# Kernel optimization log

Hardware: AMD Instinct MI355X
Metric: run time of the kernel (lower is better)

Reference implementation:

```python
import jax, jax.numpy as jnp
import numpy as np

B, N, IN_DIM, HID, K = 32, 512, 1024, 512, 3
ALPHA = 0.2  # leaky_relu negative slope
NEG = -9e15


def setup_inputs() -> dict:
    key = jax.random.key(0)
    ks = jax.random.split(key, 7)
    hidden_states = jax.random.normal(ks[0], (B, N, IN_DIM), jnp.float32)
    adj = (jax.random.uniform(ks[1], (B, 3, N, N)) < 0.05).astype(jnp.float32)
    W_all = jax.random.normal(ks[2], (3, K, IN_DIM, HID), jnp.float32) * 0.02
    a_all = jax.random.normal(ks[3], (3, K, 2 * HID, 1), jnp.float32) * 0.02
    wawa_w = jax.random.normal(ks[4], (HID, 100), jnp.float32) * 0.05
    wawa_b = jnp.zeros((100,), jnp.float32)
    ctx_w = jax.random.normal(ks[5], (100, 1), jnp.float32) * 0.05
    return {"hidden_states": hidden_states, "adj": adj, "W_all": W_all,
            "a_all": a_all, "wawa_w": wawa_w, "wawa_b": wawa_b, "ctx_w": ctx_w}


def _gat(adj_m, x, W, a):
    # e_ij = leaky_relu(cat[h_i, h_j] @ a) == leaky_relu(h_i@a1 + h_j@a2)
    h = jnp.einsum('bnf,fh->bnh', x, W)           # [B,N,HID]
    f1 = jnp.einsum('bnh,ho->bno', h, a[:HID])    # [B,N,1]
    f2 = jnp.einsum('bnh,ho->bno', h, a[HID:])    # [B,N,1]
    e = jax.nn.leaky_relu(f1 + jnp.swapaxes(f2, 1, 2), negative_slope=ALPHA)  # [B,N,N]
    att = jnp.where(adj_m > 0, e, NEG)
    att = jax.nn.softmax(att, axis=2)
    return jnp.einsum('bnm,bmh->bnh', att, h)


def reference(hidden_states, adj, W_all, a_all, wawa_w, wawa_b, ctx_w):
    adj_a, adj_b, adj_c = adj[:, 0], adj[:, 1], adj[:, 2]
    pa, pb, pc = adj_a, adj_b, adj_c  # matmuls(A, k) = A^(k+1)
    hs = []
    for layer in range(K):
        if layer > 0:
            pa = jnp.matmul(pa, adj_a)
            pb = jnp.matmul(pb, adj_b)
            pc = jnp.matmul(pc, adj_c)
        h_layer = (_gat(pa, hidden_states, W_all[0, layer], a_all[0, layer])
                   + _gat(pb, hidden_states, W_all[1, layer], a_all[1, layer])
                   + _gat(pc, hidden_states, W_all[2, layer], a_all[2, layer]))
        hs.append(h_layer)
    # attention-based combination over the K orders
    s = [jnp.einsum('bnc,co->bno', jnp.tanh(jnp.einsum('bnh,hc->bnc', h, wawa_w) + wawa_b), ctx_w)
         for h in hs]                              # each [B,N,1]
    vs = jax.nn.softmax(jnp.concatenate(s, axis=2), axis=2)  # [B,N,K]
    h_stack = jnp.stack(hs, axis=2)                # [B,N,K,HID]
    return jnp.sum(vs[..., None] * h_stack, axis=2)  # [B,N,HID]
```

## Files before the change

kernel.cpp:

```cpp
#include <hip/hip_runtime.h>
#include <hip/hip_bf16.h>

typedef short v8s __attribute__((ext_vector_type(8)));
typedef float v4f __attribute__((ext_vector_type(4)));
typedef unsigned long long u64;

#define ALPHA 0.2f

__device__ inline unsigned short f32_bf16(float x){
    unsigned int u = __float_as_uint(x);
    unsigned int r = (u + 0x7fffu + ((u >> 16) & 1u)) >> 16;
    return (unsigned short)r;
}
__device__ inline float bf16_f32(unsigned short s){
    return __uint_as_float(((unsigned int)s) << 16);
}
__device__ inline v4f mfma16(v8s a, v8s b, v4f c){
    return __builtin_amdgcn_mfma_f32_16x16x32_bf16(a, b, c, 0, 0, 0);
}
__device__ inline void gload16(const unsigned short* g, short* l){
    __builtin_amdgcn_global_load_lds((const __attribute__((address_space(1))) unsigned int*)g,
                                     (__attribute__((address_space(3))) unsigned int*)l,
                                     16, 0, 0);
}


__global__ void k_convert_x(const float* __restrict__ x, v8s* __restrict__ out, int n8){
    int i = blockIdx.x * 256 + threadIdx.x;
    if (i >= n8) return;
    const float4* p = (const float4*)x + (size_t)i * 2;
    float4 a = p[0], b = p[1];
    v8s r;
    r[0] = (short)f32_bf16(a.x); r[1] = (short)f32_bf16(a.y);
    r[2] = (short)f32_bf16(a.z); r[3] = (short)f32_bf16(a.w);
    r[4] = (short)f32_bf16(b.x); r[5] = (short)f32_bf16(b.y);
    r[6] = (short)f32_bf16(b.z); r[7] = (short)f32_bf16(b.w);
    out[i] = r;
}

__global__ void k_transpose_w(const float* __restrict__ W, unsigned short* __restrict__ Wt){
    __shared__ float tile[32][33];
    int g = blockIdx.z, k0 = blockIdx.x * 32, h0 = blockIdx.y * 32;
    int tx = threadIdx.x, ty = threadIdx.y;
    #pragma unroll
    for (int i = 0; i < 4; ++i)
        tile[ty + i*8][tx] = W[((size_t)g*1024 + k0 + ty + i*8)*512 + h0 + tx];
    __syncthreads();
    #pragma unroll
    for (int i = 0; i < 4; ++i){
        int h = ty + i*8;
        Wt[((size_t)g*512 + h0 + h)*1024 + k0 + tx] = f32_bf16(tile[tx][h]);
    }
}

__global__ void k_wawat(const float* __restrict__ w, unsigned short* __restrict__ wt){
    int i = blockIdx.x * 256 + threadIdx.x;
    if (i >= 128 * 512) return;
    int c = i >> 9, k = i & 511;
    wt[i] = (c < 100) ? f32_bf16(w[k*100 + c]) : (unsigned short)0;
}


__global__ __launch_bounds__(256) void k_bits(const float* __restrict__ adj,
                                              u64* __restrict__ bits){
    int row = blockIdx.x * 4 + (threadIdx.x >> 6);
    int t = row >> 14, b = (row >> 9) & 31, i = row & 511;
    const float* src = adj + (((size_t)b*3 + t)*512 + i)*512;
    int lane = threadIdx.x & 63;
    #pragma unroll
    for (int w = 0; w < 8; ++w){
        u64 word = __ballot(src[w*64 + lane] > 0.5f);
        if (lane == 0) bits[(size_t)row*8 + w] = word;
    }
}

__global__ __launch_bounds__(256) void k_boolmm(const u64* __restrict__ prev,
                                                const u64* __restrict__ base,
                                                u64* __restrict__ out){
    int row = blockIdx.x * 256 + threadIdx.x;
    if (row >= 49152) return;
    int tb = row >> 9;
    const u64* pr = prev + (size_t)row * 8;
    const u64* bb = base + ((size_t)tb << 9) * 8;
    ulonglong2 a0 = {0,0}, a1 = {0,0}, a2 = {0,0}, a3 = {0,0};
    #pragma unroll
    for (int w = 0; w < 8; ++w){
        u64 m = pr[w];
        const u64* bw = bb + (size_t)(w << 6) * 8;
        while (m){
            int k = __builtin_ctzll(m);
            m &= m - 1;
            const ulonglong2* br = (const ulonglong2*)(bw + (size_t)k * 8);
            ulonglong2 b0 = br[0], b1 = br[1], b2 = br[2], b3 = br[3];
            a0.x |= b0.x; a0.y |= b0.y;
            a1.x |= b1.x; a1.y |= b1.y;
            a2.x |= b2.x; a2.y |= b2.y;
            a3.x |= b3.x; a3.y |= b3.y;
        }
    }
    ulonglong2* op = (ulonglong2*)(out + (size_t)row * 8);
    op[0] = a0; op[1] = a1; op[2] = a2; op[3] = a3;
}

__global__ __launch_bounds__(256, 4) void k_gemm_h(
    const unsigned short* __restrict__ Wt, const unsigned short* __restrict__ Xb,
    unsigned short* __restrict__ Ht, const float* __restrict__ aall,
    float* __restrict__ f1p, float* __restrict__ f2p, int l)
{
    __shared__ __align__(16) short As[128*32];
    __shared__ __align__(16) short Bs[128*32];
    const int bn = blockIdx.x, bm = blockIdx.y, t = blockIdx.z;
    const int g = t*3 + l;
    const int tid = threadIdx.x;
    const int lane = tid & 63, wave = tid >> 6;
    const int wr = wave >> 1, wc = wave & 1;
    const int fr = lane & 15, fq = lane >> 4;
    const int slot = fq ^ (fr & 3) ^ ((fr >> 2) & 3);

    const int srow = tid >> 2, sw = tid & 3;
    const int gw = sw ^ (srow & 3) ^ ((srow >> 2) & 3);
    const unsigned short* Ap = Wt + ((size_t)g*512 + (size_t)bm*128 + srow)*1024 + gw*8;
    const unsigned short* Bp = Xb + ((size_t)bn*128 + srow)*1024 + gw*8;
    short* AsW = As + wave*512;
    short* BsW = Bs + wave*512;

    v4f acc[4][4] = {};

    for (int kt = 0; kt < 32; ++kt){
        const unsigned short* a0 = Ap + kt*32;
        const unsigned short* b0 = Bp + kt*32;
        gload16(a0,           AsW);
        gload16(a0 + 64*1024, AsW + 2048);
        gload16(b0,           BsW);
        gload16(b0 + 64*1024, BsW + 2048);
        __syncthreads();
        v8s af[4], bf[4];
        #pragma unroll
        for (int i = 0; i < 4; ++i) af[i] = *(const v8s*)&As[(wr*64 + i*16 + fr)*32 + slot*8];
        #pragma unroll
        for (int i = 0; i < 4; ++i) bf[i] = *(const v8s*)&Bs[(wc*64 + i*16 + fr)*32 + slot*8];
        #pragma unroll
        for (int i = 0; i < 4; ++i)
            #pragma unroll
            for (int j = 0; j < 4; ++j)
                acc[i][j] = mfma16(af[i], bf[j], acc[i][j]);
        __syncthreads();
    }
    #pragma unroll
    for (int i = 0; i < 4; ++i){
        const int h = bm*128 + wr*64 + i*16 + fq*4;
        #pragma unroll
        for (int j = 0; j < 4; ++j){
            const int mc = bn*128 + wc*64 + j*16 + fr;
            unsigned short* dst = Ht + ((size_t)t*512 + h)*16384 + mc;
            #pragma unroll
            for (int rg = 0; rg < 4; ++rg)
                dst[(size_t)rg*16384] = f32_bf16(acc[i][j][rg]);
        }
    }
    const float* a1 = aall + ((size_t)t*3 + l)*1024;
    const float* a2 = a1 + 512;
    float s1[4] = {0.f,0.f,0.f,0.f}, s2[4] = {0.f,0.f,0.f,0.f};
    #pragma unroll
    for (int i = 0; i < 4; ++i){
        #pragma unroll
        for (int rg = 0; rg < 4; ++rg){
            const int h = bm*128 + wr*64 + i*16 + fq*4 + rg;
            const float c1 = a1[h], c2 = a2[h];
            #pragma unroll
            for (int j = 0; j < 4; ++j){
                s1[j] += acc[i][j][rg]*c1;
                s2[j] += acc[i][j][rg]*c2;
            }
        }
    }
    #pragma unroll
    for (int j = 0; j < 4; ++j){
        s1[j] += __shfl_xor(s1[j], 16); s1[j] += __shfl_xor(s1[j], 32);
        s2[j] += __shfl_xor(s2[j], 16); s2[j] += __shfl_xor(s2[j], 32);
    }
    float* scr = (float*)As;
    __syncthreads();
    if (fq == 0){
        #pragma unroll
        for (int j = 0; j < 4; ++j){
            scr[(((wr*2 + wc)*4 + j)*16 + fr)*2 + 0] = s1[j];
            scr[(((wr*2 + wc)*4 + j)*16 + fr)*2 + 1] = s2[j];
        }
    }
    __syncthreads();
    if (tid < 256){
        const int which = tid & 1, fr2 = (tid >> 1) & 15, j2 = (tid >> 5) & 3,
                  wc2 = (tid >> 7) & 1;
        const float v = scr[(((0*2 + wc2)*4 + j2)*16 + fr2)*2 + which]
                      + scr[(((1*2 + wc2)*4 + j2)*16 + fr2)*2 + which];
        const int m = bn*128 + wc2*64 + j2*16 + fr2;
        float* dst = which ? f2p : f1p;
        dst[((size_t)bm*3 + t)*16384 + m] = v;
    }
}

__global__ __launch_bounds__(256) void k_f1red(
    const float* __restrict__ f1p, const float* __restrict__ f2p,
    float* __restrict__ f1, float* __restrict__ f2)
{
    int idx = blockIdx.x * 256 + threadIdx.x;
    if (idx >= 49152) return;
    float s1 = 0.f, s2 = 0.f;
    #pragma unroll
    for (int bm = 0; bm < 4; ++bm){
        int t = idx >> 14, m = idx & 16383;
        s1 += f1p[((size_t)bm*3 + t)*16384 + m];
        s2 += f2p[((size_t)bm*3 + t)*16384 + m];
    }
    f1[idx] = s1; f2[idx] = s2;
}

__device__ inline void softmax_row(int t, int b, int rt, int r, int q,
    const float* __restrict__ f1a, const float* __restrict__ f2a,
    const u64* __restrict__ maskP, float* p)
{
    const float f1v = f1a[t*16384 + b*512 + rt*64 + r];
    const u64 mw = maskP[(((size_t)t*32 + b)*512 + rt*64 + r)*8 + q];
    const float4* f2p = (const float4*)(f2a + t*16384 + b*512 + q*64);
    float sm = 0.f;
    #pragma unroll
    for (int w = 0; w < 16; ++w){
        float4 f4 = f2p[w];
        #pragma unroll
        for (int u2 = 0; u2 < 4; ++u2){
            int u = w*4 + u2;
            float e = f1v + ((const float*)&f4)[u2];
            e = (e >= 0.f) ? e : ALPHA*e;
            float pe = ((mw >> u) & 1ull) ? __expf(e) : 0.f;
            p[u] = pe; sm += pe;
        }
    }
    sm += __shfl_xor(sm, 1);
    sm += __shfl_xor(sm, 2);
    sm += __shfl_xor(sm, 4);
    const float rinv = 1.f / (sm + 1e-30f);
    #pragma unroll
    for (int u = 0; u < 64; ++u) p[u] *= rinv;
}

__device__ inline void store_att(short* __restrict__ attbuf, int r, int q,
                                 const float* p)
{
    #pragma unroll
    for (int j8 = 0; j8 < 8; ++j8){
        v8s pk;
        #pragma unroll
        for (int u = 0; u < 8; ++u) pk[u] = (short)f32_bf16(p[j8*8 + u]);
        const int cs = q*8 + (j8 ^ q);
        *(v8s*)&attbuf[r*520 + cs*8] = pk;
    }
}

#define PV_LOAD(buf, kknum) { \
    _Pragma("unroll") \
    for (int j = 0; j < 4; ++j) \
        buf[j] = *(const v8s*)(Hb + (size_t)(wave*64 + j*16 + fr)*16384 + (kknum)*32 + fq*8); }

#define PV_MFMA(buf) { \
    _Pragma("unroll") \
    for (int i = 0; i < 4; ++i) \
        _Pragma("unroll") \
        for (int j = 0; j < 4; ++j) \
            acc[i][j] = mfma16(af[i], buf[j], acc[i][j]); }

#define PV_BODY(ATT) { \
    _Pragma("unroll") \
    for (int kk = 0; kk < 16; ++kk){ \
        const int nx = kk + 3; \
        if (nx < 16){ \
            if (nx % 4 == 0)      { PV_LOAD(bva, nx) } \
            else if (nx % 4 == 1) { PV_LOAD(bvb, nx) } \
            else if (nx % 4 == 2) { PV_LOAD(bvc, nx) } \
            else                  { PV_LOAD(bvd, nx) } \
        } \
        v8s af[4]; \
        const int cb = kk*4 + fq; \
        const int cs = (cb & 56) | ((cb & 7) ^ ((cb >> 3) & 7)); \
        _Pragma("unroll") \
        for (int i = 0; i < 4; ++i) \
            af[i] = *(const v8s*)&ATT[(i*16 + fr)*520 + cs*8]; \
        if (kk % 4 == 0)      { PV_MFMA(bva) } \
        else if (kk % 4 == 1) { PV_MFMA(bvb) } \
        else if (kk % 4 == 2) { PV_MFMA(bvc) } \
        else                  { PV_MFMA(bvd) } \
    } }

__global__ __launch_bounds__(512, 2) void k_att_pv(
    const unsigned short* __restrict__ Ht,
    const float* __restrict__ f1a, const float* __restrict__ f2a,
    const u64* __restrict__ maskP,
    unsigned short* __restrict__ hlb)
{
    __shared__ __align__(16) short att0[64*520];
    __shared__ __align__(16) short att1[64*520];
    const int tid = threadIdx.x;
    const int lane = tid & 63, wave = tid >> 6;
    const int b = blockIdx.x, rt = blockIdx.y;
    const int r = tid >> 3, q = tid & 7;
    const int fr = lane & 15, fq = lane >> 4;
    v4f acc[4][4] = {};
    float p[64];
    v8s bva[4], bvb[4], bvc[4], bvd[4];

    const unsigned short* Hb = Ht + (size_t)b*512;

    PV_LOAD(bva, 0); PV_LOAD(bvb, 1); PV_LOAD(bvc, 2);
    softmax_row(0, b, rt, r, q, f1a, f2a, maskP, p);
    store_att(att0, r, q, p);
    __syncthreads();

    softmax_row(1, b, rt, r, q, f1a, f2a, maskP, p);
    store_att(att1, r, q, p);
    PV_BODY(att0);
    __syncthreads();

    Hb += (size_t)512*16384;
    PV_LOAD(bva, 0); PV_LOAD(bvb, 1); PV_LOAD(bvc, 2);
    softmax_row(2, b, rt, r, q, f1a, f2a, maskP, p);
    store_att(att0, r, q, p);
    PV_BODY(att1);
    __syncthreads();

    Hb += (size_t)512*16384;
    PV_LOAD(bva, 0); PV_LOAD(bvb, 1); PV_LOAD(bvc, 2);
    PV_BODY(att0);

    #pragma unroll
    for (int i = 0; i < 4; ++i){
        const int row = rt*64 + i*16 + fq*4;
        #pragma unroll
        for (int j = 0; j < 4; ++j){
            const int col = wave*64 + j*16 + fr;
            unsigned short* d1 = hlb + ((size_t)b*512 + row)*512 + col;
            #pragma unroll
            for (int rg = 0; rg < 4; ++rg)
                d1[(size_t)rg*512] = f32_bf16(acc[i][j][rg]);
        }
    }
}

__global__ __launch_bounds__(256) void k_gemm_s(
    const unsigned short* __restrict__ Hb, const unsigned short* __restrict__ Wwt,
    const float* __restrict__ wb, const float* __restrict__ cw,
    float* __restrict__ s)
{
    __shared__ __align__(16) short As[128*32];
    __shared__ __align__(16) short Bs[128*32];
    const int bm = blockIdx.x;
    const int tid = threadIdx.x;
    const int lane = tid & 63, wave = tid >> 6;
    const int wr = wave >> 1, wc = wave & 1;
    const int fr = lane & 15, fq = lane >> 4;
    const int slot = fq ^ (fr & 3) ^ ((fr >> 2) & 3);
    const int srow = tid >> 2, sw = tid & 3;
    const int gw = sw ^ (srow & 3) ^ ((srow >> 2) & 3);
    const unsigned short* Ap = Hb + ((size_t)bm*128 + srow)*512 + gw*8;
    const unsigned short* Bp = Wwt + (size_t)srow*512 + gw*8;

    v4f acc[4][4] = {};
    v8s ra0 = *(const v8s*)(Ap);
    v8s ra1 = *(const v8s*)(Ap + 64*512);
    v8s rb0 = *(const v8s*)(Bp);
    v8s rb1 = *(const v8s*)(Bp + 64*512);

    for (int kt = 0; kt < 16; ++kt){
        __syncthreads();
        *(v8s*)&As[tid*8]        = ra0;
        *(v8s*)&As[tid*8 + 2048] = ra1;
        *(v8s*)&Bs[tid*8]        = rb0;
        *(v8s*)&Bs[tid*8 + 2048] = rb1;
        __syncthreads();
        if (kt + 1 < 16){
            const unsigned short* An = Ap + (kt+1)*32;
            const unsigned short* Bn = Bp + (kt+1)*32;
            ra0 = *(const v8s*)(An); ra1 = *(const v8s*)(An + 64*512);
            rb0 = *(const v8s*)(Bn); rb1 = *(const v8s*)(Bn + 64*512);
        }
        v8s af[4], bf[4];
        #pragma unroll
        for (int i = 0; i < 4; ++i) af[i] = *(const v8s*)&As[(wr*64 + i*16 + fr)*32 + slot*8];
        #pragma unroll
        for (int i = 0; i < 4; ++i) bf[i] = *(const v8s*)&Bs[(wc*64 + i*16 + fr)*32 + slot*8];
        #pragma unroll
        for (int i = 0; i < 4; ++i)
            #pragma unroll
            for (int j = 0; j < 4; ++j)
                acc[i][j] = mfma16(af[i], bf[j], acc[i][j]);
    }
    float part[4][4];
    #pragma unroll
    for (int i = 0; i < 4; ++i)
        #pragma unroll
        for (int rg = 0; rg < 4; ++rg) part[i][rg] = 0.f;
    #pragma unroll
    for (int j = 0; j < 4; ++j){
        const int c = wc*64 + j*16 + fr;
        const bool valid = (c < 100);
        const float wbc = valid ? wb[c] : 0.f;
        const float cwc = valid ? cw[c] : 0.f;
        #pragma unroll
        for (int i = 0; i < 4; ++i)
            #pragma unroll
            for (int rg = 0; rg < 4; ++rg){
                float x = acc[i][j][rg] + wbc;
                float th;
                if (x > 15.f) th = 1.f;
                else if (x < -15.f) th = -1.f;
                else { float ex = __expf(2.f*x); th = (ex - 1.f) / (ex + 1.f); }
                part[i][rg] += th * cwc;
            }
    }
    #pragma unroll
    for (int i = 0; i < 4; ++i)
        #pragma unroll
        for (int rg = 0; rg < 4; ++rg){
            float v = part[i][rg];
            v += __shfl_xor(v, 1);
            v += __shfl_xor(v, 2);
            v += __shfl_xor(v, 4);
            v += __shfl_xor(v, 8);
            part[i][rg] = v;
        }
    float* scr = (float*)As;
    __syncthreads();
    if (fr == 0){
        #pragma unroll
        for (int i = 0; i < 4; ++i)
            #pragma unroll
            for (int rg = 0; rg < 4; ++rg)
                scr[(wr*64 + i*16 + fq*4 + rg)*2 + wc] = part[i][rg];
    }
    __syncthreads();
    if (tid < 128){
        const float v = scr[tid*2] + scr[tid*2 + 1];
        const int grow = bm*128 + tid;
        s[grow] = v;
    }
}

__global__ void k_sv2(const float* __restrict__ s, float* __restrict__ v)
{
    int m = blockIdx.x * 256 + threadIdx.x;
    if (m >= 16384) return;
    float s0 = s[m], s1 = s[16384 + m], s2 = s[32768 + m];
    float m0 = fmaxf(s0, fmaxf(s1, s2));
    float e0 = __expf(s0-m0), e1 = __expf(s1-m0), e2 = __expf(s2-m0);
    float inv = 1.f / (e0 + e1 + e2);
    v[m] = e0*inv; v[16384 + m] = e1*inv; v[32768 + m] = e2*inv;
}

__global__ void k_comb(const unsigned short* __restrict__ hlb, const float* __restrict__ v,
                       float* __restrict__ out)
{
    int idx = blockIdx.x * 256 + threadIdx.x;
    if (idx >= 16384*64) return;
    int m = idx >> 6, c8 = (idx & 63) << 3;
    const unsigned short* hp = hlb + (size_t)m*512 + c8;
    v8s a = *(const v8s*)hp;
    v8s bb = *(const v8s*)(hp + (size_t)16384*512);
    v8s cc = *(const v8s*)(hp + (size_t)2*16384*512);
    float v0 = v[m], v1 = v[16384+m], v2 = v[32768+m];
    float o[8];
    #pragma unroll
    for (int u = 0; u < 8; ++u)
        o[u] = v0*bf16_f32((unsigned short)a[u])
             + v1*bf16_f32((unsigned short)bb[u])
             + v2*bf16_f32((unsigned short)cc[u]);
    float4* dst = (float4*)(out + (size_t)m*512 + c8);
    dst[0] = make_float4(o[0], o[1], o[2], o[3]);
    dst[1] = make_float4(o[4], o[5], o[6], o[7]);
}

extern "C" void kernel_launch(void* const* d_in, const int* in_sizes, int n_in,
                              void* d_out, int out_size, void* d_ws, size_t ws_size,
                              hipStream_t stream)
{
    (void)in_sizes; (void)n_in; (void)out_size; (void)ws_size;
    const float* hs   = (const float*)d_in[0];
    const float* adj  = (const float*)d_in[1];
    const float* W    = (const float*)d_in[2];
    const float* aall = (const float*)d_in[3];
    const float* ww   = (const float*)d_in[4];
    const float* wb   = (const float*)d_in[5];
    const float* cw   = (const float*)d_in[6];
    float* out = (float*)d_out;
    char* ws = (char*)d_ws;

    unsigned short* Xb  = (unsigned short*)(ws);
    unsigned short* Wt  = (unsigned short*)(ws + 33554432);
    unsigned short* Wwt = (unsigned short*)(ws + 42991616);
    u64* bits           = (u64*)(ws + 43122688);
    u64* P2             = (u64*)(ws + 46268416);
    u64* P3             = (u64*)(ws + 49414144);
    unsigned short* Ht  = (unsigned short*)(ws + 52559872);
    float* f1           = (float*)(ws + 102891520);
    float* f2           = (float*)(ws + 103088128);
    float* f1p          = (float*)(ws + 103284736);
    float* f2p          = (float*)(ws + 104071168);
    unsigned short* hlb = (unsigned short*)(ws + 203948032);
    float* sbuf         = (float*)(ws + 52559872);
    float* vv           = (float*)(ws + 102891520);

    k_convert_x<<<8192, 256, 0, stream>>>(hs, (v8s*)Xb, 2097152);
    k_transpose_w<<<dim3(32,16,9), dim3(32,8), 0, stream>>>(W, Wt);
    k_wawat<<<256, 256, 0, stream>>>(ww, Wwt);
    k_bits<<<12288, 256, 0, stream>>>(adj, bits);
    k_boolmm<<<192, 256, 0, stream>>>(bits, bits, P2);
    k_boolmm<<<192, 256, 0, stream>>>(bits, P2, P3);

    const u64* masks[3] = {bits, P2, P3};
    for (int l = 0; l < 3; ++l){
        k_gemm_h<<<dim3(128,4,3), 256, 0, stream>>>(Wt, Xb, Ht, aall, f1p, f2p, l);
        k_f1red<<<192, 256, 0, stream>>>(f1p, f2p, f1, f2);
        k_att_pv<<<dim3(32,8), 512, 0, stream>>>(Ht, f1, f2, masks[l],
            hlb + (size_t)l*16384*512);
    }
    k_gemm_s<<<384, 256, 0, stream>>>(hlb, Wwt, wb, cw, sbuf);
    k_sv2<<<64, 256, 0, stream>>>(sbuf, vv);
    k_comb<<<4096, 256, 0, stream>>>(hlb, vv, out);
}
```

Measured before the change: 549.1 us.

## Split fused softmax+PV kernel into separate softmax and tiled LDS GEMM kernels

Replaces the fused attention kernel, which ran only 256 blocks of 512 threads with the softmax held in registers and LDS, with two kernels. A standalone softmax kernel writes bf16 attention rows to global memory. A 128x128-tiled MFMA GEMM then loads att and Ht into LDS via global_load_lds across 512 blocks. The aim is more parallelism and occupancy in the PV matmul, at the cost of a round trip of the attention matrix through global memory and an extra launch per layer.

```diff
diff --git a/kernel.cpp b/kernel.cpp
--- a/kernel.cpp
+++ b/kernel.cpp
@@ -216,128 +216,87 @@
     f1[idx] = s1; f2[idx] = s2;
 }
 
-__device__ inline void softmax_row(int t, int b, int rt, int r, int q,
+__global__ __launch_bounds__(256) void k_soft(
     const float* __restrict__ f1a, const float* __restrict__ f2a,
-    const u64* __restrict__ maskP, float* p)
-{
-    const float f1v = f1a[t*16384 + b*512 + rt*64 + r];
-    const u64 mw = maskP[(((size_t)t*32 + b)*512 + rt*64 + r)*8 + q];
-    const float4* f2p = (const float4*)(f2a + t*16384 + b*512 + q*64);
+    const u64* __restrict__ maskP, unsigned short* __restrict__ att)
+{
+    const int row = blockIdx.x * 4 + (threadIdx.x >> 6);
+    const int lane = threadIdx.x & 63;
+    const int tb = row >> 9;
+    const int t = tb >> 5, b = tb & 31;
+    const float f1v = f1a[t*16384 + b*512 + (row & 511)];
+    const u64 mword = maskP[(size_t)row*8 + (lane >> 3)];
+    const unsigned int mbits = (unsigned int)((mword >> ((lane & 7)*8)) & 0xffu);
+    const float4* f2p = (const float4*)(f2a + t*16384 + b*512 + lane*8);
+    float4 fa = f2p[0], fb = f2p[1];
+    float p[8];
     float sm = 0.f;
     #pragma unroll
-    for (int w = 0; w < 16; ++w){
-        float4 f4 = f2p[w];
-        #pragma unroll
-        for (int u2 = 0; u2 < 4; ++u2){
-            int u = w*4 + u2;
-            float e = f1v + ((const float*)&f4)[u2];
-            e = (e >= 0.f) ? e : ALPHA*e;
-            float pe = ((mw >> u) & 1ull) ? __expf(e) : 0.f;
-            p[u] = pe; sm += pe;
-        }
-    }
-    sm += __shfl_xor(sm, 1);
-    sm += __shfl_xor(sm, 2);
-    sm += __shfl_xor(sm, 4);
+    for (int u = 0; u < 8; ++u){
+        float e = f1v + ((u < 4) ? ((const float*)&fa)[u] : ((const float*)&fb)[u-4]);
+        e = (e >= 0.f) ? e : ALPHA*e;
+        float pe = (mbits & (1u << u)) ? __expf(e) : 0.f;
+        p[u] = pe; sm += pe;
+    }
+    sm += __shfl_xor(sm, 1);  sm += __shfl_xor(sm, 2);  sm += __shfl_xor(sm, 4);
+    sm += __shfl_xor(sm, 8);  sm += __shfl_xor(sm, 16); sm += __shfl_xor(sm, 32);
     const float rinv = 1.f / (sm + 1e-30f);
-    #pragma unroll
-    for (int u = 0; u < 64; ++u) p[u] *= rinv;
-}
-
-__device__ inline void store_att(short* __restrict__ attbuf, int r, int q,
-                                 const float* p)
-{
-    #pragma unroll
-    for (int j8 = 0; j8 < 8; ++j8){
-        v8s pk;
-        #pragma unroll
-        for (int u = 0; u < 8; ++u) pk[u] = (short)f32_bf16(p[j8*8 + u]);
-        const int cs = q*8 + (j8 ^ q);
-        *(v8s*)&attbuf[r*520 + cs*8] = pk;
-    }
-}
-
-#define PV_LOAD(buf, kknum) { \
-    _Pragma("unroll") \
-    for (int j = 0; j < 4; ++j) \
-        buf[j] = *(const v8s*)(Hb + (size_t)(wave*64 + j*16 + fr)*16384 + (kknum)*32 + fq*8); }
-
-#define PV_MFMA(buf) { \
-    _Pragma("unroll") \
-    for (int i = 0; i < 4; ++i) \
-        _Pragma("unroll") \
-        for (int j = 0; j < 4; ++j) \
-            acc[i][j] = mfma16(af[i], buf[j], acc[i][j]); }
-
-#define PV_BODY(ATT) { \
-    _Pragma("unroll") \
-    for (int kk = 0; kk < 16; ++kk){ \
-        const int nx = kk + 3; \
-        if (nx < 16){ \
-            if (nx % 4 == 0)      { PV_LOAD(bva, nx) } \
-            else if (nx % 4 == 1) { PV_LOAD(bvb, nx) } \
-            else if (nx % 4 == 2) { PV_LOAD(bvc, nx) } \
-            else                  { PV_LOAD(bvd, nx) } \
-        } \
-        v8s af[4]; \
-        const int cb = kk*4 + fq; \
-        const int cs = (cb & 56) | ((cb & 7) ^ ((cb >> 3) & 7)); \
-        _Pragma("unroll") \
-        for (int i = 0; i < 4; ++i) \
-            af[i] = *(const v8s*)&ATT[(i*16 + fr)*520 + cs*8]; \
-        if (kk % 4 == 0)      { PV_MFMA(bva) } \
-        else if (kk % 4 == 1) { PV_MFMA(bvb) } \
-        else if (kk % 4 == 2) { PV_MFMA(bvc) } \
-        else                  { PV_MFMA(bvd) } \
-    } }
-
-__global__ __launch_bounds__(512, 2) void k_att_pv(
-    const unsigned short* __restrict__ Ht,
-    const float* __restrict__ f1a, const float* __restrict__ f2a,
-    const u64* __restrict__ maskP,
+    v8s pk;
+    #pragma unroll
+    for (int u = 0; u < 8; ++u) pk[u] = (short)f32_bf16(p[u] * rinv);
+    *(v8s*)&att[(size_t)row*512 + lane*8] = pk;
+}
+
+__global__ __launch_bounds__(256, 4) void k_pv(
+    const unsigned short* __restrict__ att, const unsigned short* __restrict__ Ht,
     unsigned short* __restrict__ hlb)
 {
-    __shared__ __align__(16) short att0[64*520];
-    __shared__ __align__(16) short att1[64*520];
+    __shared__ __align__(16) short As[128*32];
+    __shared__ __align__(16) short Bs[128*32];
+    const int hc = blockIdx.x, rt = blockIdx.y, b = blockIdx.z;
     const int tid = threadIdx.x;
     const int lane = tid & 63, wave = tid >> 6;
-    const int b = blockIdx.x, rt = blockIdx.y;
-    const int r = tid >> 3, q = tid & 7;
+    const int wr = wave >> 1, wc = wave & 1;
     const int fr = lane & 15, fq = lane >> 4;
+    const int slot = fq ^ (fr & 3) ^ ((fr >> 2) & 3);
+    const int srow = tid >> 2, sw = tid & 3;
+    const int gw = sw ^ (srow & 3) ^ ((srow >> 2) & 3);
+    short* AsW = As + wave*512;
+    short* BsW = Bs + wave*512;
+
     v4f acc[4][4] = {};
-    float p[64];
-    v8s bva[4], bvb[4], bvc[4], bvd[4];
-
-    const unsigned short* Hb = Ht + (size_t)b*512;
-
-    PV_LOAD(bva, 0); PV_LOAD(bvb, 1); PV_LOAD(bvc, 2);
-    softmax_row(0, b, rt, r, q, f1a, f2a, maskP, p);
-    store_att(att0, r, q, p);
-    __syncthreads();
-
-    softmax_row(1, b, rt, r, q, f1a, f2a, maskP, p);
-    store_att(att1, r, q, p);
-    PV_BODY(att0);
-    __syncthreads();
-
-    Hb += (size_t)512*16384;
-    PV_LOAD(bva, 0); PV_LOAD(bvb, 1); PV_LOAD(bvc, 2);
-    softmax_row(2, b, rt, r, q, f1a, f2a, maskP, p);
-    store_att(att0, r, q, p);
-    PV_BODY(att1);
-    __syncthreads();
-
-    Hb += (size_t)512*16384;
-    PV_LOAD(bva, 0); PV_LOAD(bvb, 1); PV_LOAD(bvc, 2);
-    PV_BODY(att0);
-
+
+    for (int t = 0; t < 3; ++t){
+        const unsigned short* Ap = att + ((size_t)((t*32 + b)*512 + rt*128 + srow))*512 + gw*8;
+        const unsigned short* Bp = Ht + ((size_t)t*512 + hc*128 + srow)*16384 + (size_t)b*512 + gw*8;
+        for (int kk = 0; kk < 16; ++kk){
+            const unsigned short* a0 = Ap + kk*32;
+            const unsigned short* b0 = Bp + kk*32;
+            gload16(a0,                    AsW);
+            gload16(a0 + 64*512,           AsW + 2048);
+            gload16(b0,                    BsW);
+            gload16(b0 + (size_t)64*16384, BsW + 2048);
+            __syncthreads();
+            v8s af[4], bf[4];
+            #pragma unroll
+            for (int i = 0; i < 4; ++i) af[i] = *(const v8s*)&As[(wr*64 + i*16 + fr)*32 + slot*8];
+            #pragma unroll
+            for (int j = 0; j < 4; ++j) bf[j] = *(const v8s*)&Bs[(wc*64 + j*16 + fr)*32 + slot*8];
+            #pragma unroll
+            for (int i = 0; i < 4; ++i)
+                #pragma unroll
+                for (int j = 0; j < 4; ++j)
+                    acc[i][j] = mfma16(af[i], bf[j], acc[i][j]);
+            __syncthreads();
+        }
+    }
     #pragma unroll
     for (int i = 0; i < 4; ++i){
-        const int row = rt*64 + i*16 + fq*4;
+        const int r = rt*128 + wr*64 + i*16 + fq*4;
         #pragma unroll
         for (int j = 0; j < 4; ++j){
-            const int col = wave*64 + j*16 + fr;
-            unsigned short* d1 = hlb + ((size_t)b*512 + row)*512 + col;
+            const int h = hc*128 + wc*64 + j*16 + fr;
+            unsigned short* d1 = hlb + ((size_t)b*512 + r)*512 + h;
             #pragma unroll
             for (int rg = 0; rg < 4; ++rg)
                 d1[(size_t)rg*512] = f32_bf16(acc[i][j][rg]);
@@ -503,6 +462,7 @@
     float* f2           = (float*)(ws + 103088128);
     float* f1p          = (float*)(ws + 103284736);
     float* f2p          = (float*)(ws + 104071168);
+    unsigned short* att = (unsigned short*)(ws + 104857600);
     unsigned short* hlb = (unsigned short*)(ws + 203948032);
     float* sbuf         = (float*)(ws + 52559872);
     float* vv           = (float*)(ws + 102891520);
@@ -518,7 +478,8 @@
     for (int l = 0; l < 3; ++l){
         k_gemm_h<<<dim3(128,4,3), 256, 0, stream>>>(Wt, Xb, Ht, aall, f1p, f2p, l);
         k_f1red<<<192, 256, 0, stream>>>(f1p, f2p, f1, f2);
-        k_att_pv<<<dim3(32,8), 512, 0, stream>>>(Ht, f1, f2, masks[l],
+        k_soft<<<12288, 256, 0, stream>>>(f1, f2, masks[l], att);
+        k_pv<<<dim3(4,4,32), 256, 0, stream>>>(att, Ht,
             hlb + (size_t)l*16384*512);
     }
     k_gemm_s<<<384, 256, 0, stream>>>(hlb, Wwt, wb, cw, sbuf);
```

Result: faster. 528.7 us (-3.7%).
